# Kernel optimization log

Hardware: AMD Instinct MI355X
Metric: run time of the kernel (lower is better)

Reference implementation:

```python
import jax, jax.numpy as jnp
import numpy as np

B, N, DIM = 8, 4096, 512
HEADS, DIM_HEAD = 8, 64
HIDDEN = HEADS * DIM_HEAD
SCALE = DIM_HEAD ** -0.5
NEG = -1e15


def setup_inputs() -> dict:
    key = jax.random.key(0)
    k1, k2, k3, k4, k5 = jax.random.split(key, 5)
    x = jax.random.normal(k1, (B, N, DIM), dtype=jnp.float32)
    lengths = jax.random.randint(k2, (B,), 1, N + 1, dtype=jnp.int64) if jax.config.jax_enable_x64 else jax.random.randint(k2, (B,), 1, N + 1, dtype=jnp.int32)
    w_qkv = jax.random.normal(k3, (3 * HIDDEN, DIM), dtype=jnp.float32) * 0.02
    w_out = jax.random.normal(k4, (DIM, HIDDEN), dtype=jnp.float32) * 0.02
    b_out = jax.random.normal(k5, (DIM,), dtype=jnp.float32) * 0.02
    return {"x": x, "w_qkv": w_qkv, "w_out": w_out, "b_out": b_out, "lengths": lengths}


def reference(x, w_qkv, w_out, b_out, lengths):
    b, n, dim = x.shape
    # positions >= length are masked (equivalent to the cumsum trick in torch)
    pos = jnp.arange(n)
    seq_mask = pos[None, :] >= lengths[:, None]  # (b, n), True => padding

    x = jnp.where(seq_mask[:, :, None], 0.0, x)

    # pointwise Conv1d == matmul over channel dim; channels are head-major
    qkv = jnp.einsum('bnd,ed->bne', x, w_qkv)  # (b, n, 3*hidden)
    q, k, v = jnp.split(qkv, 3, axis=-1)

    def to_heads(t):  # (b, n, hidden) -> (b, heads, dim_head, n)
        return t.reshape(b, n, HEADS, DIM_HEAD).transpose(0, 2, 3, 1)

    q, k, v = to_heads(q), to_heads(k), to_heads(v)
    q = q * SCALE

    m = seq_mask[:, None, None, :]  # (b, 1, 1, n)
    q = jnp.where(m, 0.0, q)
    k = jnp.where(m, NEG, k)
    k = jax.nn.softmax(k, axis=-1)  # softmax over sequence

    context = jnp.einsum('bhdn,bhen->bhde', k, v)   # (b, h, d, d)
    out = jnp.einsum('bhde,bhdn->bhen', context, q)  # (b, h, d, n)
    out = out.transpose(0, 1, 2, 3).reshape(b, HIDDEN, n)  # (b, hidden, n), head-major
    out = jnp.einsum('bcn,dc->bdn', out, w_out) + b_out[None, :, None]
    return out.transpose(0, 2, 1)  # (b, n, dim)
```

## Files before the change

kernel.cpp:

```cpp
#include <hip/hip_runtime.h>

typedef unsigned short u16;
typedef unsigned int u32;
typedef __bf16 bf16x8 __attribute__((ext_vector_type(8)));
typedef float f32x4 __attribute__((ext_vector_type(4)));

#define L2E 1.44269504088896340736f

static __device__ __forceinline__ u16 f2bf(float f) {
  u32 u = __float_as_uint(f);
  u32 r = (u + 0x7fffu + ((u >> 16) & 1u)) >> 16;
  return (u16)r;
}
static __device__ __forceinline__ float bf2f(u32 bits) {
  return __uint_as_float(bits << 16);
}
static __device__ __forceinline__ u32 trunc_bf(float f) {
  return __float_as_uint(f) >> 16;
}

__global__ __launch_bounds__(256) void cvt_x(const float* __restrict__ src,
                                             u16* __restrict__ dst,
                                             const int* __restrict__ lengths) {
  int i = (blockIdx.x * 256 + threadIdx.x) * 8;
  int row = i >> 9;
  if ((row & 4095) >= lengths[row >> 12]) return;
  float4 a = *(const float4*)(src + i);
  float4 b = *(const float4*)(src + i + 4);
  union { u16 h[8]; uint4 v; } o;
  o.h[0] = f2bf(a.x); o.h[1] = f2bf(a.y); o.h[2] = f2bf(a.z); o.h[3] = f2bf(a.w);
  o.h[4] = f2bf(b.x); o.h[5] = f2bf(b.y); o.h[6] = f2bf(b.z); o.h[7] = f2bf(b.w);
  *(uint4*)(dst + i) = o.v;
}

__global__ __launch_bounds__(256) void prep_w(const float* __restrict__ w_qkv,
                                              u16* __restrict__ wqT,
                                              u16* __restrict__ wkvb) {
  __shared__ u16 tile[64][65];
  int bid = blockIdx.x;
  int t = threadIdx.x;
  if (bid < 64) {
    int c0 = (bid & 7) * 64, s0 = (bid >> 3) * 64;
    int r = t >> 4, cc = (t & 15) * 4;
#pragma unroll
    for (int i = 0; i < 4; ++i) {
      int row = r + i * 16;
      float4 v = *(const float4*)(w_qkv + (size_t)(c0 + row) * 512 + s0 + cc);
      tile[row][cc] = f2bf(v.x); tile[row][cc + 1] = f2bf(v.y);
      tile[row][cc + 2] = f2bf(v.z); tile[row][cc + 3] = f2bf(v.w);
    }
    __syncthreads();
#pragma unroll
    for (int i = 0; i < 4; ++i) {
      int srow = r + i * 16;
      union { u16 h[4]; uint2 u; } pk;
#pragma unroll
      for (int j = 0; j < 4; ++j) pk.h[j] = tile[cc + j][srow];
      *(uint2*)(wqT + (size_t)(s0 + srow) * 512 + c0 + cc) = pk.u;
    }
  } else {
    int i = ((bid - 64) * 256 + t) * 8;
    const float* src = w_qkv + 262144;
    float4 a = *(const float4*)(src + i);
    float4 b = *(const float4*)(src + i + 4);
    union { u16 h[8]; uint4 v; } o;
    o.h[0] = f2bf(a.x); o.h[1] = f2bf(a.y); o.h[2] = f2bf(a.z); o.h[3] = f2bf(a.w);
    o.h[4] = f2bf(b.x); o.h[5] = f2bf(b.y); o.h[6] = f2bf(b.z); o.h[7] = f2bf(b.w);
    *(uint4*)(wkvb + i) = o.v;
  }
}

template <int MODE>
__global__ __launch_bounds__(256, 4) void gemm128(const u16* __restrict__ A,
                                                  const u16* __restrict__ Bm,
                                                  u16* __restrict__ outb,
                                                  float* __restrict__ outf,
                                                  const float* __restrict__ bias,
                                                  const int* __restrict__ lengths) {
  __shared__ u16 lA[8192];
  __shared__ u16 lB[8192];

  const int t = threadIdx.x;
  const int w = t >> 6, lane = t & 63, lm = lane & 15, lg = lane >> 4;
  const int wr = w >> 1, wc = w & 1;
  const int col0 = blockIdx.y * 128;

  int row0, L = 0, myb = -1;
  if constexpr (MODE == 1) {
    row0 = blockIdx.x * 128;
  } else {
    const int pid = blockIdx.x;
    int na[8], pref = 0, panel = 0;
#pragma unroll
    for (int b = 0; b < 8; ++b) {
      int Lb = lengths[b];
      na[b] = (Lb + 127) >> 7;
      if (myb < 0 && pid < pref + na[b]) { myb = b; panel = pid - pref; L = Lb; }
      pref += na[b];
    }
    if (myb < 0) {
      if constexpr (MODE == 0) return;
      int pid2 = pid - pref, pm = 0;
#pragma unroll
      for (int b = 0; b < 8; ++b) {
        int mb = 32 - na[b];
        if (myb < 0 && pid2 < pm + mb) { myb = b; panel = na[b] + pid2 - pm; }
        pm += mb;
      }
      row0 = myb * 4096 + panel * 128;
      for (int i = t; i < 4096; i += 256) {
        int r = i >> 5, c = (i & 31) * 4;
        *(f32x4*)(outf + (size_t)(row0 + r) * 512 + col0 + c) =
            *(const f32x4*)(bias + col0 + c);
      }
      return;
    }
    row0 = myb * 4096 + panel * 128;
  }

  const u16* Abase = A + (size_t)row0 * 512;
  const u16* Bbase = Bm + (size_t)col0 * 512;
  if constexpr (MODE == 2) Bbase += (size_t)myb * 262144;

  size_t goff[4];
#pragma unroll
  for (int i = 0; i < 4; ++i) {
    int c = i * 256 + t, r = c >> 3, s = (c & 7) ^ (r & 7);
    goff[i] = (size_t)r * 512 + s * 8;
  }

  const int swz0 = (lg ^ (lm & 7)) * 8;
  const int swz1 = ((4 + lg) ^ (lm & 7)) * 8;

  f32x4 acc[4][4] = {};

  for (int kt = 0; kt < 8; ++kt) {
    const u16* sa = Abase + kt * 64;
    const u16* sb = Bbase + kt * 64;
#pragma unroll
    for (int i = 0; i < 4; ++i)
      __builtin_amdgcn_global_load_lds(
          (const __attribute__((address_space(1))) void*)(sa + goff[i]),
          (__attribute__((address_space(3))) void*)(&lA[(i * 256 + w * 64) * 8]),
          16, 0, 0);
#pragma unroll
    for (int i = 0; i < 4; ++i)
      __builtin_amdgcn_global_load_lds(
          (const __attribute__((address_space(1))) void*)(sb + goff[i]),
          (__attribute__((address_space(3))) void*)(&lB[(i * 256 + w * 64) * 8]),
          16, 0, 0);
    __syncthreads();

    const u16* la = &lA[(wr * 64 + lm) * 64];
    const u16* lb = &lB[(wc * 64 + lm) * 64];
    bf16x8 bfr[2][4];
#pragma unroll
    for (int nf = 0; nf < 4; ++nf) {
      bfr[0][nf] = *(const bf16x8*)(lb + nf * 1024 + swz0);
      bfr[1][nf] = *(const bf16x8*)(lb + nf * 1024 + swz1);
    }
#pragma unroll
    for (int mf = 0; mf < 4; ++mf) {
      bf16x8 af0 = *(const bf16x8*)(la + mf * 1024 + swz0);
      bf16x8 af1 = *(const bf16x8*)(la + mf * 1024 + swz1);
      __builtin_amdgcn_s_setprio(1);
#pragma unroll
      for (int nf = 0; nf < 4; ++nf) {
        acc[mf][nf] = __builtin_amdgcn_mfma_f32_16x16x32_bf16(
            bfr[0][nf], af0, acc[mf][nf], 0, 0, 0);
        acc[mf][nf] = __builtin_amdgcn_mfma_f32_16x16x32_bf16(
            bfr[1][nf], af1, acc[mf][nf], 0, 0, 0);
      }
      __builtin_amdgcn_s_setprio(0);
    }
    __syncthreads();
  }

  if constexpr (MODE == 0) {
    const int cls = col0 >> 9;
#pragma unroll
    for (int mf = 0; mf < 4; ++mf) {
      int grow = row0 + wr * 64 + mf * 16 + lm;
      int n = grow & 4095, bb = grow >> 12;
      bool msk = (n >= L);
#pragma unroll
      for (int nf = 0; nf < 4; ++nf) {
        int c = col0 + wc * 64 + nf * 16 + lg * 4;
        int h = (c >> 6) & 7;
        int off = (cls == 0) ? (c & 63) : (64 + (c & 63));
        f32x4 v = acc[mf][nf];
        if (msk) {
          float mv = (cls == 0) ? -1e15f : 0.f;
          v[0] = mv; v[1] = mv; v[2] = mv; v[3] = mv;
        }
        union { u16 h4[4]; uint2 u; } pk;
        pk.h4[0] = f2bf(v[0]); pk.h4[1] = f2bf(v[1]);
        pk.h4[2] = f2bf(v[2]); pk.h4[3] = f2bf(v[3]);
        *(uint2*)(outb + ((size_t)((bb * 8 + h) * 4096 + n)) * 128 + off) = pk.u;
      }
    }
  } else if constexpr (MODE == 1) {
#pragma unroll
    for (int mf = 0; mf < 4; ++mf) {
      int grow = row0 + wr * 64 + mf * 16 + lm;
      u16* rp = outb + (size_t)grow * 512 + col0 + wc * 64 + lg * 4;
#pragma unroll
      for (int nf = 0; nf < 4; ++nf) {
        f32x4 v = acc[mf][nf];
        union { u16 h4[4]; uint2 u; } pk;
        pk.h4[0] = f2bf(v[0]); pk.h4[1] = f2bf(v[1]);
        pk.h4[2] = f2bf(v[2]); pk.h4[3] = f2bf(v[3]);
        *(uint2*)(rp + nf * 16) = pk.u;
      }
    }
  } else {
    f32x4 b4[4];
#pragma unroll
    for (int nf = 0; nf < 4; ++nf)
      b4[nf] = *(const f32x4*)(bias + col0 + wc * 64 + nf * 16 + lg * 4);
#pragma unroll
    for (int mf = 0; mf < 4; ++mf) {
      int grow = row0 + wr * 64 + mf * 16 + lm;
      bool msk = ((grow & 4095) >= L);
      float* rp = outf + (size_t)grow * 512 + col0 + wc * 64 + lg * 4;
#pragma unroll
      for (int nf = 0; nf < 4; ++nf) {
        f32x4 v = msk ? b4[nf] : (acc[mf][nf] + b4[nf]);
        *(f32x4*)(rp + nf * 16) = v;
      }
    }
  }
}

struct CtxGrp {
  bf16x8 praw[2][2], vraw[2][2];
};

static __device__ __forceinline__ void ctx_load(const u16* __restrict__ base, int g,
                                                int lm, int lg, CtxGrp& X) {
  const u16* rp = base + (size_t)(g * 32 + lm) * 128 + lg * 8;
#pragma unroll
  for (int mt = 0; mt < 2; ++mt)
#pragma unroll
    for (int dh = 0; dh < 2; ++dh) {
      const u16* p = rp + mt * 2048 + dh * 32;
      X.praw[mt][dh] = *(const bf16x8*)(p);
      X.vraw[mt][dh] = *(const bf16x8*)(p + 64);
    }
}

static __device__ __forceinline__ void ctx_compute(const CtxGrp& X, bf16x8 I1, bf16x8 I2,
                                                   f32x4 acc[4][4], float sacc[4]) {
  const f32x4 zero = {0.f, 0.f, 0.f, 0.f};
  bf16x8 pf[2][2];
#pragma unroll
  for (int mt = 0; mt < 2; ++mt)
#pragma unroll
    for (int dh = 0; dh < 2; ++dh) {
      union { bf16x8 v; u32 w4[4]; } in;
      in.v = X.praw[mt][dh];
      union { u16 h[8]; bf16x8 v; } o;
#pragma unroll
      for (int i = 0; i < 4; ++i) {
        float a = bf2f(in.w4[i] & 0xffffu) * L2E;
        float bq = bf2f(in.w4[i] >> 16) * L2E;
        o.h[2 * i] = f2bf(exp2f(a));
        o.h[2 * i + 1] = f2bf(exp2f(bq));
      }
      pf[mt][dh] = o.v;
    }

  f32x4 tP[2][4], tV[2][4];
#pragma unroll
  for (int mt = 0; mt < 2; ++mt)
#pragma unroll
    for (int dh = 0; dh < 2; ++dh) {
      tP[mt][dh * 2] = __builtin_amdgcn_mfma_f32_16x16x32_bf16(pf[mt][dh], I1, zero, 0, 0, 0);
      tP[mt][dh * 2 + 1] = __builtin_amdgcn_mfma_f32_16x16x32_bf16(pf[mt][dh], I2, zero, 0, 0, 0);
      tV[mt][dh * 2] = __builtin_amdgcn_mfma_f32_16x16x32_bf16(X.vraw[mt][dh], I1, zero, 0, 0, 0);
      tV[mt][dh * 2 + 1] = __builtin_amdgcn_mfma_f32_16x16x32_bf16(X.vraw[mt][dh], I2, zero, 0, 0, 0);
    }

#pragma unroll
  for (int dt = 0; dt < 4; ++dt)
#pragma unroll
    for (int mt = 0; mt < 2; ++mt)
      sacc[dt] += tP[mt][dt][0] + tP[mt][dt][1] + tP[mt][dt][2] + tP[mt][dt][3];

  bf16x8 A2[4], B2[4];
#pragma unroll
  for (int dt = 0; dt < 4; ++dt) {
    union { u32 w4[4]; bf16x8 v; } a, bb2;
#pragma unroll
    for (int mt = 0; mt < 2; ++mt) {
      a.w4[mt * 2] = trunc_bf(tP[mt][dt][0]) | (trunc_bf(tP[mt][dt][1]) << 16);
      a.w4[mt * 2 + 1] = trunc_bf(tP[mt][dt][2]) | (trunc_bf(tP[mt][dt][3]) << 16);
      bb2.w4[mt * 2] = trunc_bf(tV[mt][dt][0]) | (trunc_bf(tV[mt][dt][1]) << 16);
      bb2.w4[mt * 2 + 1] = trunc_bf(tV[mt][dt][2]) | (trunc_bf(tV[mt][dt][3]) << 16);
    }
    A2[dt] = a.v; B2[dt] = bb2.v;
  }

#pragma unroll
  for (int dt = 0; dt < 4; ++dt)
#pragma unroll
    for (int et = 0; et < 4; ++et)
      acc[dt][et] = __builtin_amdgcn_mfma_f32_16x16x32_bf16(A2[dt], B2[et], acc[dt][et], 0, 0, 0);
}

__global__ __launch_bounds__(256) void ctx_gemm(const u16* __restrict__ kvh,
                                                float* __restrict__ ctxp,
                                                float* __restrict__ csum,
                                                const int* __restrict__ lengths) {
  int chunk = blockIdx.x;
  int bh = blockIdx.y;
  int b = bh >> 3;
  int L = lengths[b];
  int rows = L - chunk * 512;
  if (rows <= 0) return;

  int t = threadIdx.x;
  int w = t >> 6, lane = t & 63, lm = lane & 15, lg = lane >> 4;

  int wrows = rows - w * 128;
  int ngw = (wrows <= 0) ? 0 : (wrows >= 128 ? 4 : ((wrows + 31) >> 5));

  __shared__ float red[4][4096];
  __shared__ float redc[4][64];

  bf16x8 I1, I2;
  {
    union { u16 h[8]; bf16x8 v; } u1, u2;
#pragma unroll
    for (int j = 0; j < 8; ++j) {
      u1.h[j] = (lg * 8 + j == lm) ? 0x3F80 : 0;
      u2.h[j] = (lg * 8 + j == lm + 16) ? 0x3F80 : 0;
    }
    I1 = u1.v; I2 = u2.v;
  }

  f32x4 acc[4][4] = {};
  float sacc[4] = {};

  const u16* base = kvh + ((size_t)bh * 4096 + (size_t)chunk * 512 + (size_t)w * 128) * 128;

  for (int g = 0; g < ngw; ++g) {
    CtxGrp X;
    ctx_load(base, g, lm, lg, X);
    ctx_compute(X, I1, I2, acc, sacc);
  }

#pragma unroll
  for (int dt = 0; dt < 4; ++dt)
#pragma unroll
    for (int et = 0; et < 4; ++et)
#pragma unroll
      for (int r = 0; r < 4; ++r)
        red[w][(dt * 16 + lg * 4 + r) * 64 + et * 16 + lm] = acc[dt][et][r];
#pragma unroll
  for (int dt = 0; dt < 4; ++dt) {
    float s = sacc[dt];
    s += __shfl_xor(s, 16);
    s += __shfl_xor(s, 32);
    if (lg == 0) redc[w][dt * 16 + lm] = s;
  }
  __syncthreads();

  float* outp = ctxp + ((size_t)bh * 8 + chunk) * 4096;
#pragma unroll
  for (int j = 0; j < 4; ++j) {
    int i = t * 4 + j * 1024;
    f32x4 v = *(const f32x4*)&red[0][i];
    v += *(const f32x4*)&red[1][i];
    v += *(const f32x4*)&red[2][i];
    v += *(const f32x4*)&red[3][i];
    *(f32x4*)(outp + i) = v;
  }
  if (t < 64)
    csum[((size_t)bh * 8 + chunk) * 64 + t] =
        redc[0][t] + redc[1][t] + redc[2][t] + redc[3][t];
}

__global__ __launch_bounds__(256) void reduce_ctx(const float* __restrict__ ctxp,
                                                  float* __restrict__ ctxr,
                                                  const int* __restrict__ lengths) {
  int blk = blockIdx.x;
  int bh = blk >> 2, s = blk & 3;
  int nch = (lengths[bh >> 3] + 511) >> 9;
  int i = s * 1024 + threadIdx.x * 4;
  const float* p = ctxp + (size_t)bh * 8 * 4096 + i;
  f32x4 acc = {0.f, 0.f, 0.f, 0.f};
  for (int ch = 0; ch < nch; ++ch) acc += *(const f32x4*)(p + (size_t)ch * 4096);
  *(f32x4*)(ctxr + (size_t)bh * 4096 + i) = acc;
}

__global__ __launch_bounds__(256) void m_gemm(const float* __restrict__ ctxr,
                                              const float* __restrict__ csum,
                                              const float* __restrict__ w_out,
                                              u16* __restrict__ MT,
                                              const int* __restrict__ lengths) {
  int bh = blockIdx.x;
  int grp = blockIdx.y;
  int b = bh >> 3, h = bh & 7;
  int nch = (lengths[b] + 511) >> 9;
  int dd0 = grp * 128;
  int t = threadIdx.x;
  __shared__ short sctx[64 * 64];
  __shared__ short sw[128 * 64];
  {
    const float* cp = ctxr + (size_t)bh * 4096;
    int i0 = t * 16;
    int d = t >> 2;
    float den = 0.f;
    for (int ch = 0; ch < nch; ++ch) den += csum[((size_t)bh * 8 + ch) * 64 + d];
    float rin = 1.0f / den;
#pragma unroll
    for (int j = 0; j < 16; j += 4) {
      float4 v = *(const float4*)(cp + i0 + j);
      sctx[i0 + j] = (short)f2bf(v.x * rin);
      sctx[i0 + j + 1] = (short)f2bf(v.y * rin);
      sctx[i0 + j + 2] = (short)f2bf(v.z * rin);
      sctx[i0 + j + 3] = (short)f2bf(v.w * rin);
    }
  }
  {
#pragma unroll
    for (int j = 0; j < 32; j += 4) {
      int idx = t * 32 + j;
      int row = idx >> 6, col = idx & 63;
      float4 v = *(const float4*)(w_out + (size_t)(dd0 + row) * 512 + h * 64 + col);
      sw[idx] = (short)f2bf(v.x); sw[idx + 1] = (short)f2bf(v.y);
      sw[idx + 2] = (short)f2bf(v.z); sw[idx + 3] = (short)f2bf(v.w);
    }
  }
  __syncthreads();

  int lane = t & 63, w = t >> 6;
  int lm = lane & 15, lk = (lane >> 4) * 8;
  f32x4 acc[2][4] = {};
#pragma unroll
  for (int kk = 0; kk < 2; ++kk) {
    bf16x8 af[2], bfr[4];
#pragma unroll
    for (int mb = 0; mb < 2; ++mb)
      af[mb] = *(const bf16x8*)(sw + (w * 32 + mb * 16 + lm) * 64 + kk * 32 + lk);
#pragma unroll
    for (int nb = 0; nb < 4; ++nb)
      bfr[nb] = *(const bf16x8*)(sctx + (nb * 16 + lm) * 64 + kk * 32 + lk);
#pragma unroll
    for (int mb = 0; mb < 2; ++mb)
#pragma unroll
      for (int nb = 0; nb < 4; ++nb)
        acc[mb][nb] = __builtin_amdgcn_mfma_f32_16x16x32_bf16(af[mb], bfr[nb], acc[mb][nb], 0, 0, 0);
  }
  u16* outp = MT + (size_t)b * 512 * 512;
#pragma unroll
  for (int mb = 0; mb < 2; ++mb)
#pragma unroll
    for (int r = 0; r < 4; ++r) {
      int dd = dd0 + w * 32 + mb * 16 + (lane >> 4) * 4 + r;
#pragma unroll
      for (int nb = 0; nb < 4; ++nb) {
        int c = h * 64 + nb * 16 + lm;
        outp[dd * 512 + c] = f2bf(acc[mb][nb][r] * 0.125f);
      }
    }
}

extern "C" void kernel_launch(void* const* d_in, const int* in_sizes, int n_in,
                              void* d_out, int out_size, void* d_ws, size_t ws_size,
                              hipStream_t stream) {
  const float* x = (const float*)d_in[0];
  const float* w_qkv = (const float*)d_in[1];
  const float* w_out = (const float*)d_in[2];
  const float* b_out = (const float*)d_in[3];
  const int* lengths = (const int*)d_in[4];
  float* out = (float*)d_out;
  char* ws = (char*)d_ws;

  u16* kvh    = (u16*)(ws);
  u16* xb     = (u16*)(ws + 67108864);
  u16* wkvb   = (u16*)(ws + 100663296);
  u16* wqT    = (u16*)(ws + 101711872);
  float* ctxp = (float*)(ws + 102236160);
  float* csum = (float*)(ws + 110624768);
  float* ctxr = (float*)(ws + 110755840);
  u16* MT     = (u16*)(ws + 111804416);
  u16* G      = (u16*)(ws + 115998720);

  cvt_x<<<8192, 256, 0, stream>>>(x, xb, lengths);
  prep_w<<<320, 256, 0, stream>>>(w_qkv, wqT, wkvb);
  gemm128<0><<<dim3(256, 8), 256, 0, stream>>>(xb, wkvb, kvh, nullptr, nullptr, lengths);
  ctx_gemm<<<dim3(8, 64), 256, 0, stream>>>(kvh, ctxp, csum, lengths);
  reduce_ctx<<<256, 256, 0, stream>>>(ctxp, ctxr, lengths);
  m_gemm<<<dim3(64, 4), 256, 0, stream>>>(ctxr, csum, w_out, MT, lengths);
  gemm128<1><<<dim3(32, 4), 256, 0, stream>>>(MT, wqT, G, nullptr, nullptr, nullptr);
  gemm128<2><<<dim3(256, 4), 256, 0, stream>>>(xb, G, nullptr, out, b_out, lengths);
}
```

Baseline: 107.8 us.

## Add dedicated 256-row KV projection GEMM with per-head interleaved weight layout

Replaces the generic 128x128 gemm128<0> for the K/V projection with a new kv_gemm kernel that uses 512 threads and 256-row A tiles. prep_w now reorders the K and V weight rows so that each head's 64 K rows and 64 V rows sit next to each other. Each block then produces the full 128-wide K|V slab for one head, and the epilogue writes contiguous rows into the head-major kvh buffer. This raises A-tile reuse and makes the output stores contiguous, at the cost of more LDS per block and fewer blocks, which could lower occupancy and leave tail work unbalanced across panels of varying length.

```diff
diff --git a/kernel.cpp b/kernel.cpp
--- a/kernel.cpp
+++ b/kernel.cpp
@@ -60,13 +60,128 @@
     }
   } else {
     int i = ((bid - 64) * 256 + t) * 8;
+    int row = i >> 9, col = i & 511;
+    int drow;
+    if (row < 512) drow = (row >> 6) * 128 + (row & 63);
+    else { int r2 = row - 512; drow = (r2 >> 6) * 128 + 64 + (r2 & 63); }
     const float* src = w_qkv + 262144;
     float4 a = *(const float4*)(src + i);
     float4 b = *(const float4*)(src + i + 4);
     union { u16 h[8]; uint4 v; } o;
     o.h[0] = f2bf(a.x); o.h[1] = f2bf(a.y); o.h[2] = f2bf(a.z); o.h[3] = f2bf(a.w);
     o.h[4] = f2bf(b.x); o.h[5] = f2bf(b.y); o.h[6] = f2bf(b.z); o.h[7] = f2bf(b.w);
-    *(uint4*)(wkvb + i) = o.v;
+    *(uint4*)(wkvb + (size_t)drow * 512 + col) = o.v;
+  }
+}
+
+__global__ __launch_bounds__(512, 4) void kv_gemm(const u16* __restrict__ A,
+                                                  const u16* __restrict__ Bm,
+                                                  u16* __restrict__ kvh,
+                                                  const int* __restrict__ lengths) {
+  __shared__ u16 lA[16384];
+  __shared__ u16 lB[8192];
+
+  const int t = threadIdx.x;
+  const int w = t >> 6, lane = t & 63, lm = lane & 15, lg = lane >> 4;
+  const int wr = w >> 1, wc = w & 1;
+  const int h = blockIdx.y;
+
+  int row0, L = 0, myb = -1, panel = 0;
+  {
+    const int pid = blockIdx.x;
+    int pref = 0;
+#pragma unroll
+    for (int b = 0; b < 8; ++b) {
+      int Lb = lengths[b];
+      int nb = (Lb + 255) >> 8;
+      if (myb < 0 && pid < pref + nb) { myb = b; panel = pid - pref; L = Lb; }
+      pref += nb;
+    }
+    if (myb < 0) return;
+    row0 = myb * 4096 + panel * 256;
+  }
+
+  const u16* Abase = A + (size_t)row0 * 512;
+  const u16* Bbase = Bm + (size_t)h * 128 * 512;
+
+  size_t aoff[4], boff[2];
+#pragma unroll
+  for (int i = 0; i < 4; ++i) {
+    int c = i * 512 + t, r = c >> 3, s = (c & 7) ^ (r & 7);
+    aoff[i] = (size_t)r * 512 + s * 8;
+  }
+#pragma unroll
+  for (int i = 0; i < 2; ++i) {
+    int c = i * 512 + t, r = c >> 3, s = (c & 7) ^ (r & 7);
+    boff[i] = (size_t)r * 512 + s * 8;
+  }
+
+  const int swz0 = (lg ^ (lm & 7)) * 8;
+  const int swz1 = ((4 + lg) ^ (lm & 7)) * 8;
+
+  f32x4 acc[4][4] = {};
+
+  for (int kt = 0; kt < 8; ++kt) {
+    const u16* sa = Abase + kt * 64;
+    const u16* sb = Bbase + kt * 64;
+#pragma unroll
+    for (int i = 0; i < 4; ++i)
+      __builtin_amdgcn_global_load_lds(
+          (const __attribute__((address_space(1))) void*)(sa + aoff[i]),
+          (__attribute__((address_space(3))) void*)(&lA[(i * 512 + w * 64) * 8]),
+          16, 0, 0);
+#pragma unroll
+    for (int i = 0; i < 2; ++i)
+      __builtin_amdgcn_global_load_lds(
+          (const __attribute__((address_space(1))) void*)(sb + boff[i]),
+          (__attribute__((address_space(3))) void*)(&lB[(i * 512 + w * 64) * 8]),
+          16, 0, 0);
+    __syncthreads();
+
+    const u16* la = &lA[(wr * 64 + lm) * 64];
+    const u16* lb = &lB[(wc * 64 + lm) * 64];
+    bf16x8 bfr[2][4];
+#pragma unroll
+    for (int nf = 0; nf < 4; ++nf) {
+      bfr[0][nf] = *(const bf16x8*)(lb + nf * 1024 + swz0);
+      bfr[1][nf] = *(const bf16x8*)(lb + nf * 1024 + swz1);
+    }
+#pragma unroll
+    for (int mf = 0; mf < 4; ++mf) {
+      bf16x8 af0 = *(const bf16x8*)(la + mf * 1024 + swz0);
+      bf16x8 af1 = *(const bf16x8*)(la + mf * 1024 + swz1);
+      __builtin_amdgcn_s_setprio(1);
+#pragma unroll
+      for (int nf = 0; nf < 4; ++nf) {
+        acc[mf][nf] = __builtin_amdgcn_mfma_f32_16x16x32_bf16(
+            bfr[0][nf], af0, acc[mf][nf], 0, 0, 0);
+        acc[mf][nf] = __builtin_amdgcn_mfma_f32_16x16x32_bf16(
+            bfr[1][nf], af1, acc[mf][nf], 0, 0, 0);
+      }
+      __builtin_amdgcn_s_setprio(0);
+    }
+    __syncthreads();
+  }
+
+#pragma unroll
+  for (int mf = 0; mf < 4; ++mf) {
+    int grow = row0 + wr * 64 + mf * 16 + lm;
+    int n = grow & 4095;
+    bool msk = (n >= L);
+    u16* rp = kvh + ((size_t)((myb * 8 + h) * 4096 + n)) * 128 + wc * 64 + lg * 4;
+#pragma unroll
+    for (int nf = 0; nf < 4; ++nf) {
+      int c = wc * 64 + nf * 16 + lg * 4;
+      f32x4 v = acc[mf][nf];
+      if (msk) {
+        float mv = (c < 64) ? -1e15f : 0.f;
+        v[0] = mv; v[1] = mv; v[2] = mv; v[3] = mv;
+      }
+      union { u16 h4[4]; uint2 u; } pk;
+      pk.h4[0] = f2bf(v[0]); pk.h4[1] = f2bf(v[1]);
+      pk.h4[2] = f2bf(v[2]); pk.h4[3] = f2bf(v[3]);
+      *(uint2*)(rp + nf * 16) = pk.u;
+    }
   }
 }
 
@@ -99,7 +214,6 @@
       pref += na[b];
     }
     if (myb < 0) {
-      if constexpr (MODE == 0) return;
       int pid2 = pid - pref, pm = 0;
 #pragma unroll
       for (int b = 0; b < 8; ++b) {
@@ -176,30 +290,7 @@
     __syncthreads();
   }
 
-  if constexpr (MODE == 0) {
-    const int cls = col0 >> 9;
-#pragma unroll
-    for (int mf = 0; mf < 4; ++mf) {
-      int grow = row0 + wr * 64 + mf * 16 + lm;
-      int n = grow & 4095, bb = grow >> 12;
-      bool msk = (n >= L);
-#pragma unroll
-      for (int nf = 0; nf < 4; ++nf) {
-        int c = col0 + wc * 64 + nf * 16 + lg * 4;
-        int h = (c >> 6) & 7;
-        int off = (cls == 0) ? (c & 63) : (64 + (c & 63));
-        f32x4 v = acc[mf][nf];
-        if (msk) {
-          float mv = (cls == 0) ? -1e15f : 0.f;
-          v[0] = mv; v[1] = mv; v[2] = mv; v[3] = mv;
-        }
-        union { u16 h4[4]; uint2 u; } pk;
-        pk.h4[0] = f2bf(v[0]); pk.h4[1] = f2bf(v[1]);
-        pk.h4[2] = f2bf(v[2]); pk.h4[3] = f2bf(v[3]);
-        *(uint2*)(outb + ((size_t)((bb * 8 + h) * 4096 + n)) * 128 + off) = pk.u;
-      }
-    }
-  } else if constexpr (MODE == 1) {
+  if constexpr (MODE == 1) {
 #pragma unroll
     for (int mf = 0; mf < 4; ++mf) {
       int grow = row0 + wr * 64 + mf * 16 + lm;
@@ -490,7 +581,7 @@
 
   cvt_x<<<8192, 256, 0, stream>>>(x, xb, lengths);
   prep_w<<<320, 256, 0, stream>>>(w_qkv, wqT, wkvb);
-  gemm128<0><<<dim3(256, 8), 256, 0, stream>>>(xb, wkvb, kvh, nullptr, nullptr, lengths);
+  kv_gemm<<<dim3(128, 8), 512, 0, stream>>>(xb, wkvb, kvh, lengths);
   ctx_gemm<<<dim3(8, 64), 256, 0, stream>>>(kvh, ctxp, csum, lengths);
   reduce_ctx<<<256, 256, 0, stream>>>(ctxp, ctxr, lengths);
   m_gemm<<<dim3(64, 4), 256, 0, stream>>>(ctxr, csum, w_out, MT, lengths);
```

Result: slower. 118.4 us (+9.9%).
